# Optimization experiments

Hardware: AMD Instinct MI355X
Metric: run time of the kernel (lower is better)

## Reference

```python
import jax, jax.numpy as jnp
import numpy as np

N_HEAD = 16

def setup_inputs() -> dict:
    key = jax.random.key(0)
    ks = jax.random.split(key, 5)
    C = 1024
    s = 0.02
    return {
        "x": jax.random.normal(ks[0], (4, 2048, C), dtype=jnp.float32),
        "w_attn": jax.random.normal(ks[1], (C, 3 * C), dtype=jnp.float32) * s,
        "b_attn": jnp.zeros((3 * C,), dtype=jnp.float32),
        "w_proj": jax.random.normal(ks[2], (C, C), dtype=jnp.float32) * s,
        "b_proj": jnp.zeros((C,), dtype=jnp.float32),
    }

def reference(x, w_attn, b_attn, w_proj, b_proj):
    B, T, C = x.shape
    H = N_HEAD
    D = C // H
    qkv = x @ w_attn + b_attn                      # [B,T,3C]
    q, k, v = jnp.split(qkv, 3, axis=-1)
    # [B,H,T,D]
    q = q.reshape(B, T, H, D).transpose(0, 2, 1, 3)
    k = k.reshape(B, T, H, D).transpose(0, 2, 1, 3)
    v = v.reshape(B, T, H, D).transpose(0, 2, 1, 3)
    scale = 1.0 / np.sqrt(D).astype(np.float32)
    attn = jnp.einsum('bhtd,bhsd->bhts', q, k) * scale   # [B,H,T,T]
    causal = jnp.tril(jnp.ones((T, T), dtype=bool))
    attn = jnp.where(causal, attn, -jnp.inf)
    attn = jax.nn.softmax(attn, axis=-1)
    y = jnp.einsum('bhts,bhsd->bhtd', attn, v)           # [B,H,T,D]
    y = y.transpose(0, 2, 1, 3).reshape(B, T, C)
    return y @ w_proj + b_proj
```

## Files before the change

### kernel.cpp

```cpp
#include <hip/hip_runtime.h>
#include <hip/hip_bf16.h>

typedef short short8 __attribute__((ext_vector_type(8)));
typedef float f32x4 __attribute__((ext_vector_type(4)));
typedef float f32x16 __attribute__((ext_vector_type(16)));

typedef __attribute__((address_space(1))) void as1_void;
typedef __attribute__((address_space(3))) void as3_void;

__device__ __forceinline__ unsigned short f2bf(float f) {
    __hip_bfloat16 h = __float2bfloat16(f);
    return __builtin_bit_cast(unsigned short, h);
}

__device__ __forceinline__ float exp2fast(float x) {
    return __builtin_amdgcn_exp2f(x);
}

__device__ __forceinline__ unsigned int cvtpk(float lo, float hi) {
    unsigned int r;
    asm("v_cvt_pk_bf16_f32 %0, %1, %2" : "=v"(r) : "v"(lo), "v"(hi));
    return r;
}

__device__ __forceinline__ void plswap(unsigned int& a, unsigned int& b) {
    asm("v_permlane32_swap_b32 %0, %1" : "+v"(a), "+v"(b));
}

__device__ __forceinline__ void gload16(const unsigned short* g, unsigned short* l) {
    __builtin_amdgcn_global_load_lds((as1_void*)g, (as3_void*)l, 16, 0, 0);
}

__global__ __launch_bounds__(256) void conv_f32_to_bf16(
    const float* __restrict__ in, unsigned short* __restrict__ out, int n4) {
    int i = blockIdx.x * 256 + threadIdx.x;
    if (i >= n4) return;
    float4 v = ((const float4*)in)[i];
    ushort4 o;
    o.x = f2bf(v.x); o.y = f2bf(v.y); o.z = f2bf(v.z); o.w = f2bf(v.w);
    ((ushort4*)out)[i] = o;
}

__global__ __launch_bounds__(256) void transpose_f32_to_bf16(
    const float* __restrict__ W, unsigned short* __restrict__ WT, int K, int N) {
    __shared__ float tile[32][33];
    int tx = threadIdx.x, ty = threadIdx.y;
    int n0 = blockIdx.x * 32, k0 = blockIdx.y * 32;
#pragma unroll
    for (int j = 0; j < 4; ++j)
        tile[ty + j * 8][tx] = W[(size_t)(k0 + ty + j * 8) * N + n0 + tx];
    __syncthreads();
#pragma unroll
    for (int j = 0; j < 4; ++j)
        WT[(size_t)(n0 + ty + j * 8) * K + k0 + tx] = f2bf(tile[tx][ty + j * 8]);
}

template <int MODE>
__global__ __launch_bounds__(256, 2) void gemm_bt(
    const unsigned short* __restrict__ A,
    const unsigned short* __restrict__ Bt,
    const float* __restrict__ bias,
    void* __restrict__ out0,
    unsigned short* __restrict__ out1,
    int M, int N, int K) {
    __shared__ unsigned short sA[128 * 32];
    __shared__ unsigned short sB[128 * 32];
    const int tid = threadIdx.x;
    const int lane = tid & 63;
    const int w = tid >> 6;
    const int wr = (w >> 1) * 64;
    const int wc = (w & 1) * 64;
    const size_t arow0 = (size_t)blockIdx.x * 128;
    const size_t brow0 = (size_t)blockIdx.y * 128;

    const int grow = (w << 5) + (lane >> 2);
    const int gcol = (lane & 3) << 3;
    const unsigned short* pA0 = A + (arow0 + grow) * (size_t)K + gcol;
    const unsigned short* pB0 = Bt + (brow0 + grow) * (size_t)K + gcol;
    unsigned short* lA = sA + (w << 10);
    unsigned short* lB = sB + (w << 10);

    f32x4 acc[4][4] = {};
    const int fr = lane & 15;
    const int fk = (lane >> 4) << 3;

    for (int k0 = 0; k0 < K; k0 += 32) {
        __syncthreads();
        gload16(pA0 + k0, lA);
        gload16(pA0 + 16 * (size_t)K + k0, lA + 512);
        gload16(pB0 + k0, lB);
        gload16(pB0 + 16 * (size_t)K + k0, lB + 512);
        __syncthreads();

        short8 af[4], bfr[4];
#pragma unroll
        for (int i = 0; i < 4; ++i)
            af[i] = *(const short8*)&sA[(wr + i * 16 + fr) * 32 + fk];
#pragma unroll
        for (int i = 0; i < 4; ++i)
            bfr[i] = *(const short8*)&sB[(wc + i * 16 + fr) * 32 + fk];
#pragma unroll
        for (int mi = 0; mi < 4; ++mi)
#pragma unroll
            for (int ni = 0; ni < 4; ++ni)
                acc[mi][ni] = __builtin_amdgcn_mfma_f32_16x16x32_bf16(
                    af[mi], bfr[ni], acc[mi][ni], 0, 0, 0);
    }

    const int fq = (lane >> 4) << 2;
    if constexpr (MODE == 0) {
#pragma unroll
        for (int mi = 0; mi < 4; ++mi)
#pragma unroll
            for (int ni = 0; ni < 4; ++ni) {
                size_t r = arow0 + wr + mi * 16 + fq;
                size_t c = brow0 + wc + ni * 16 + fr;
                float bv = bias[c];
#pragma unroll
                for (int j = 0; j < 4; ++j)
                    ((float*)out0)[(r + j) * (size_t)N + c] = acc[mi][ni][j] + bv;
            }
    } else {
        const bool isv = (int)(brow0 + wc) >= 2048;
        if (isv) {
#pragma unroll
            for (int mi = 0; mi < 4; ++mi)
#pragma unroll
                for (int ni = 0; ni < 4; ++ni) {
                    int c = (int)brow0 + wc + ni * 16 + fr;
                    float bv = bias[c];
                    int cv = c - 2048;
                    int r0 = (int)arow0 + wr + mi * 16 + fq;
                    int bb = r0 >> 11, t0 = r0 & 2047;
                    unsigned int lo = (unsigned int)f2bf(acc[mi][ni][0] + bv) |
                                      ((unsigned int)f2bf(acc[mi][ni][1] + bv) << 16);
                    unsigned int hi = (unsigned int)f2bf(acc[mi][ni][2] + bv) |
                                      ((unsigned int)f2bf(acc[mi][ni][3] + bv) << 16);
                    *(uint2*)&out1[(((size_t)(bb * 1024 + cv)) << 11) + t0] =
                        make_uint2(lo, hi);
                }
        } else {
            const float qs = ((int)(brow0 + wc) < 1024) ? 0.125f * 1.4426950408889634f
                                                        : 1.0f;
#pragma unroll
            for (int mi = 0; mi < 4; ++mi)
#pragma unroll
                for (int ni = 0; ni < 4; ++ni) {
                    size_t r = arow0 + wr + mi * 16 + fq;
                    size_t c = brow0 + wc + ni * 16 + fr;
                    float bv = bias[c];
#pragma unroll
                    for (int j = 0; j < 4; ++j)
                        ((unsigned short*)out0)[(r + j) * 2048 + c] =
                            f2bf((acc[mi][ni][j] + bv) * qs);
                }
        }
    }
}

__global__ __launch_bounds__(256, 2) void attn_mfma(
    const unsigned short* __restrict__ qk,
    const unsigned short* __restrict__ vt,
    unsigned short* __restrict__ y,
    int BH) {
    constexpr int T = 2048;
    constexpr float THR = 8.0f;

    __shared__ __align__(16) unsigned short sK[2][64 * 64];
    __shared__ __align__(16) unsigned short sV[2][64 * 64];

    const int tid = threadIdx.x;
    const int lane = tid & 63;
    const int w = tid >> 6;
    const int l31 = lane & 31;
    const int b5 = lane >> 5;

    const int bh = blockIdx.x % BH;
    const int qt = 15 - blockIdx.x / BH;
    const int b = bh >> 4;
    const int h = bh & 15;
    const int q0 = qt << 7;
    const int qw0 = q0 + w * 32;

    const unsigned short* kbase = qk + ((size_t)(b * T)) * 2048 + 1024 + h * 64;
    const unsigned short* vbase = vt + ((size_t)(b * 1024 + h * 64)) * 2048;

    const int srow = tid >> 3;
    const int c16 = tid & 7;
    const int swz = ((c16 ^ (srow & 7)) << 3);

    short8 vones;
#pragma unroll
    for (int i = 0; i < 8; ++i) vones[i] = (short)0x3F80;

    short8 aq[4];
    {
        const unsigned short* qbase =
            qk + ((size_t)(b * T + qw0 + l31)) * 2048 + h * 64;
#pragma unroll
        for (int kc = 0; kc < 4; ++kc)
            aq[kc] = *(const short8*)(qbase + b5 * 8 + kc * 16);
    }

    f32x16 O0 = {}, O1 = {};
    f32x16 l_st = {};
    float m_st = -1e30f;

    const int nt = (q0 + 128) >> 6;

    uint4 kd0, kd1, vd0, vd1;
    kd0 = *(const uint4*)(kbase + (size_t)(srow) * 2048 + c16 * 8);
    kd1 = *(const uint4*)(kbase + (size_t)(srow + 32) * 2048 + c16 * 8);
    vd0 = *(const uint4*)(vbase + (size_t)srow * 2048 + c16 * 8);
    vd1 = *(const uint4*)(vbase + (size_t)(srow + 32) * 2048 + c16 * 8);
    *(uint4*)&sK[0][srow * 64 + swz] = kd0;
    *(uint4*)&sK[0][(srow + 32) * 64 + swz] = kd1;
    *(uint4*)&sV[0][srow * 64 + swz] = vd0;
    *(uint4*)&sV[0][(srow + 32) * 64 + swz] = vd1;
    __syncthreads();

    int cur = 0;
    for (int it = 0; it < nt; ++it) {
        const int s0 = it << 6;
        const bool haveNext = (it + 1 < nt);
        if (haveNext) {
            const int s1 = s0 + 64;
            kd0 = *(const uint4*)(kbase + (size_t)(s1 + srow) * 2048 + c16 * 8);
            kd1 = *(const uint4*)(kbase + (size_t)(s1 + srow + 32) * 2048 + c16 * 8);
            vd0 = *(const uint4*)(vbase + (size_t)srow * 2048 + s1 + c16 * 8);
            vd1 = *(const uint4*)(vbase + (size_t)(srow + 32) * 2048 + s1 + c16 * 8);
        }
        const unsigned short* sKc = sK[cur];
        const unsigned short* sVc = sV[cur];

        if (s0 <= qw0 + 31) {
            f32x16 sacc[2] = {};
            __builtin_amdgcn_s_setprio(1);
#pragma unroll
            for (int kc = 0; kc < 4; ++kc) {
#pragma unroll
                for (int ni = 0; ni < 2; ++ni) {
                    const int row = ni * 32 + l31;
                    short8 akf = *(const short8*)&sKc[row * 64 +
                                                      (((b5 + kc * 2) ^ (row & 7))
                                                       << 3)];
                    sacc[ni] = __builtin_amdgcn_mfma_f32_32x32x16_bf16(
                        akf, aq[kc], sacc[ni], 0, 0, 0);
                }
            }
            __builtin_amdgcn_s_setprio(0);

            const bool needMask = (s0 + 63 > qw0);
            const int qg = qw0 + l31;
            if (needMask) {
#pragma unroll
                for (int ni = 0; ni < 2; ++ni)
#pragma unroll
                    for (int reg = 0; reg < 16; ++reg) {
                        const int sg = s0 + ni * 32 + (reg & 3) + 8 * (reg >> 2) +
                                       4 * b5;
                        sacc[ni][reg] = (sg <= qg) ? sacc[ni][reg] : -INFINITY;
                    }
            }

            float mx = sacc[0][0];
#pragma unroll
            for (int reg = 1; reg < 16; ++reg) mx = fmaxf(mx, sacc[0][reg]);
#pragma unroll
            for (int reg = 0; reg < 16; ++reg) mx = fmaxf(mx, sacc[1][reg]);
            mx = fmaxf(mx, __shfl_xor(mx, 32));

            const bool resc = __any(mx > m_st + THR);
            float f_l = 1.0f;
            if (resc) {
                const float mn = fmaxf(m_st, mx);
                f_l = exp2fast(m_st - mn);
                m_st = mn;
            }

#pragma unroll
            for (int ni = 0; ni < 2; ++ni)
#pragma unroll
                for (int reg = 0; reg < 16; ++reg)
                    sacc[ni][reg] = exp2fast(sacc[ni][reg] - m_st);

            short8 pa[4];
#pragma unroll
            for (int c = 0; c < 4; ++c) {
                const int ni = c >> 1;
                const int off = (c & 1) * 8;
                unsigned int pk01 = cvtpk(sacc[ni][off + 0], sacc[ni][off + 1]);
                unsigned int pk23 = cvtpk(sacc[ni][off + 2], sacc[ni][off + 3]);
                unsigned int pk45 = cvtpk(sacc[ni][off + 4], sacc[ni][off + 5]);
                unsigned int pk67 = cvtpk(sacc[ni][off + 6], sacc[ni][off + 7]);
                plswap(pk01, pk45);
                plswap(pk23, pk67);
                uint4 u = make_uint4(pk01, pk23, pk45, pk67);
                pa[c] = __builtin_bit_cast(short8, u);
            }

            if (resc) {
                const int fil = __builtin_bit_cast(int, f_l);
#pragma unroll
                for (int reg = 0; reg < 16; ++reg) {
                    const int qpat = (reg & 3) + 8 * (reg >> 2) + 4 * b5;
                    const float fq = __builtin_bit_cast(
                        float, __builtin_amdgcn_ds_bpermute(
                                   (qpat + (lane & 32)) << 2, fil));
                    O0[reg] *= fq;
                    O1[reg] *= fq;
                    l_st[reg] *= fq;
                }
            }

            f32x16 lacc = {};
            __builtin_amdgcn_s_setprio(1);
#pragma unroll
            for (int c = 0; c < 4; ++c) {
                lacc = __builtin_amdgcn_mfma_f32_32x32x16_bf16(
                    pa[c], vones, lacc, 0, 0, 0);
                {
                    const int row = l31;
                    short8 bvf = *(const short8*)&sVc[row * 64 +
                                                      (((c * 2 + b5) ^ (row & 7))
                                                       << 3)];
                    O0 = __builtin_amdgcn_mfma_f32_32x32x16_bf16(
                        pa[c], bvf, O0, 0, 0, 0);
                }
                {
                    const int row = 32 + l31;
                    short8 bvf = *(const short8*)&sVc[row * 64 +
                                                      (((c * 2 + b5) ^ (row & 7))
                                                       << 3)];
                    O1 = __builtin_amdgcn_mfma_f32_32x32x16_bf16(
                        pa[c], bvf, O1, 0, 0, 0);
                }
            }
            __builtin_amdgcn_s_setprio(0);
#pragma unroll
            for (int reg = 0; reg < 16; ++reg) l_st[reg] += lacc[reg];
        }

        if (haveNext) {
            unsigned short* sKn = sK[cur ^ 1];
            unsigned short* sVn = sV[cur ^ 1];
            *(uint4*)&sKn[srow * 64 + swz] = kd0;
            *(uint4*)&sKn[(srow + 32) * 64 + swz] = kd1;
            *(uint4*)&sVn[srow * 64 + swz] = vd0;
            *(uint4*)&sVn[(srow + 32) * 64 + swz] = vd1;
        }
        __syncthreads();
        cur ^= 1;
    }

#pragma unroll
    for (int reg = 0; reg < 16; ++reg) {
        const int qpat = (reg & 3) + 8 * (reg >> 2) + 4 * b5;
        const float inv = 1.0f / l_st[reg];
        const size_t base = (size_t)(b * T + qw0 + qpat) * 1024 + h * 64 + l31;
        y[base] = f2bf(O0[reg] * inv);
        y[base + 32] = f2bf(O1[reg] * inv);
    }
}

extern "C" void kernel_launch(void* const* d_in, const int* in_sizes, int n_in,
                              void* d_out, int out_size, void* d_ws, size_t ws_size,
                              hipStream_t stream) {
    const float* x      = (const float*)d_in[0];
    const float* w_attn = (const float*)d_in[1];
    const float* b_attn = (const float*)d_in[2];
    const float* w_proj = (const float*)d_in[3];
    const float* b_proj = (const float*)d_in[4];

    const int C = 1024, T = 2048, H = 16;
    const int B = in_sizes[0] / (T * C);
    const int M = B * T;

    unsigned short* xb  = (unsigned short*)d_ws;
    unsigned short* wTa = xb + (size_t)M * C;
    unsigned short* wTp = wTa + (size_t)3 * C * C;
    unsigned short* qkb = wTp + (size_t)C * C;
    unsigned short* vtb = qkb + (size_t)M * 2 * C;
    unsigned short* y   = xb;

    int n4 = (M * C) / 4;
    conv_f32_to_bf16<<<(n4 + 255) / 256, 256, 0, stream>>>(x, xb, n4);
    transpose_f32_to_bf16<<<dim3(3 * C / 32, C / 32), dim3(32, 8), 0, stream>>>(
        w_attn, wTa, C, 3 * C);
    transpose_f32_to_bf16<<<dim3(C / 32, C / 32), dim3(32, 8), 0, stream>>>(
        w_proj, wTp, C, C);
    gemm_bt<2><<<dim3(M / 128, (3 * C) / 128), 256, 0, stream>>>(
        xb, wTa, b_attn, (void*)qkb, vtb, M, 3 * C, C);
    attn_mfma<<<dim3((B * H) * 16), 256, 0, stream>>>(qkb, vtb, y, B * H);
    gemm_bt<0><<<dim3(M / 128, C / 128), 256, 0, stream>>>(
        y, wTp, b_proj, d_out, nullptr, M, C, C);
}
```

Measured before the change: 173.4 us.

## Fuse fp32-to-bf16 conversion of x into QKV GEMM A-tile loading

Removes the standalone conversion kernel for x. The QKV GEMM now reads fp32 activations straight from global memory, packs them to bf16 in registers and stores them to LDS, while B still uses direct global-to-LDS loads. Launch bounds also move from 2 to 3 waves-per-SIMD occupancy. This saves one kernel launch and a bf16 round trip through memory, at the cost of reading fp32 A data again for every N-tile (24 times) and doing the conversion in the GEMM's inner loop.

```diff
diff --git a/kernel.cpp b/kernel.cpp
--- a/kernel.cpp
+++ b/kernel.cpp
@@ -11,6 +11,9 @@
 __device__ __forceinline__ unsigned short f2bf(float f) {
     __hip_bfloat16 h = __float2bfloat16(f);
     return __builtin_bit_cast(unsigned short, h);
+}
+__device__ __forceinline__ unsigned int pack2(float a, float b) {
+    return (unsigned int)f2bf(a) | ((unsigned int)f2bf(b) << 16);
 }
 
 __device__ __forceinline__ float exp2fast(float x) {
@@ -29,16 +32,6 @@
 
 __device__ __forceinline__ void gload16(const unsigned short* g, unsigned short* l) {
     __builtin_amdgcn_global_load_lds((as1_void*)g, (as3_void*)l, 16, 0, 0);
-}
-
-__global__ __launch_bounds__(256) void conv_f32_to_bf16(
-    const float* __restrict__ in, unsigned short* __restrict__ out, int n4) {
-    int i = blockIdx.x * 256 + threadIdx.x;
-    if (i >= n4) return;
-    float4 v = ((const float4*)in)[i];
-    ushort4 o;
-    o.x = f2bf(v.x); o.y = f2bf(v.y); o.z = f2bf(v.z); o.w = f2bf(v.w);
-    ((ushort4*)out)[i] = o;
 }
 
 __global__ __launch_bounds__(256) void transpose_f32_to_bf16(
@@ -56,8 +49,8 @@
 }
 
 template <int MODE>
-__global__ __launch_bounds__(256, 2) void gemm_bt(
-    const unsigned short* __restrict__ A,
+__global__ __launch_bounds__(256, 3) void gemm_bt(
+    const void* __restrict__ A,
     const unsigned short* __restrict__ Bt,
     const float* __restrict__ bias,
     void* __restrict__ out0,
@@ -75,7 +68,9 @@
 
     const int grow = (w << 5) + (lane >> 2);
     const int gcol = (lane & 3) << 3;
-    const unsigned short* pA0 = A + (arow0 + grow) * (size_t)K + gcol;
+    const unsigned short* pA0 =
+        (const unsigned short*)A + (arow0 + grow) * (size_t)K + gcol;
+    const float* pAf = (const float*)A + (arow0 + grow) * (size_t)K + gcol;
     const unsigned short* pB0 = Bt + (brow0 + grow) * (size_t)K + gcol;
     unsigned short* lA = sA + (w << 10);
     unsigned short* lB = sB + (w << 10);
@@ -86,10 +81,25 @@
 
     for (int k0 = 0; k0 < K; k0 += 32) {
         __syncthreads();
-        gload16(pA0 + k0, lA);
-        gload16(pA0 + 16 * (size_t)K + k0, lA + 512);
-        gload16(pB0 + k0, lB);
-        gload16(pB0 + 16 * (size_t)K + k0, lB + 512);
+        if constexpr (MODE == 0) {
+            gload16(pA0 + k0, lA);
+            gload16(pA0 + 16 * (size_t)K + k0, lA + 512);
+            gload16(pB0 + k0, lB);
+            gload16(pB0 + 16 * (size_t)K + k0, lB + 512);
+        } else {
+            float4 xa0 = *(const float4*)(pAf + k0);
+            float4 xa1 = *(const float4*)(pAf + k0 + 4);
+            float4 xb0 = *(const float4*)(pAf + 16 * (size_t)K + k0);
+            float4 xb1 = *(const float4*)(pAf + 16 * (size_t)K + k0 + 4);
+            gload16(pB0 + k0, lB);
+            gload16(pB0 + 16 * (size_t)K + k0, lB + 512);
+            uint4 w0 = make_uint4(pack2(xa0.x, xa0.y), pack2(xa0.z, xa0.w),
+                                  pack2(xa1.x, xa1.y), pack2(xa1.z, xa1.w));
+            uint4 w1 = make_uint4(pack2(xb0.x, xb0.y), pack2(xb0.z, xb0.w),
+                                  pack2(xb1.x, xb1.y), pack2(xb1.z, xb1.w));
+            *(uint4*)&sA[grow * 32 + gcol] = w0;
+            *(uint4*)&sA[(grow + 16) * 32 + gcol] = w1;
+        }
         __syncthreads();
 
         short8 af[4], bfr[4];
@@ -132,10 +142,8 @@
                     int cv = c - 2048;
                     int r0 = (int)arow0 + wr + mi * 16 + fq;
                     int bb = r0 >> 11, t0 = r0 & 2047;
-                    unsigned int lo = (unsigned int)f2bf(acc[mi][ni][0] + bv) |
-                                      ((unsigned int)f2bf(acc[mi][ni][1] + bv) << 16);
-                    unsigned int hi = (unsigned int)f2bf(acc[mi][ni][2] + bv) |
-                                      ((unsigned int)f2bf(acc[mi][ni][3] + bv) << 16);
+                    unsigned int lo = pack2(acc[mi][ni][0] + bv, acc[mi][ni][1] + bv);
+                    unsigned int hi = pack2(acc[mi][ni][2] + bv, acc[mi][ni][3] + bv);
                     *(uint2*)&out1[(((size_t)(bb * 1024 + cv)) << 11) + t0] =
                         make_uint2(lo, hi);
                 }
@@ -376,22 +384,19 @@
     const int B = in_sizes[0] / (T * C);
     const int M = B * T;
 
-    unsigned short* xb  = (unsigned short*)d_ws;
-    unsigned short* wTa = xb + (size_t)M * C;
+    unsigned short* yb  = (unsigned short*)d_ws;
+    unsigned short* wTa = yb + (size_t)M * C;
     unsigned short* wTp = wTa + (size_t)3 * C * C;
     unsigned short* qkb = wTp + (size_t)C * C;
     unsigned short* vtb = qkb + (size_t)M * 2 * C;
-    unsigned short* y   = xb;
-
-    int n4 = (M * C) / 4;
-    conv_f32_to_bf16<<<(n4 + 255) / 256, 256, 0, stream>>>(x, xb, n4);
+
     transpose_f32_to_bf16<<<dim3(3 * C / 32, C / 32), dim3(32, 8), 0, stream>>>(
         w_attn, wTa, C, 3 * C);
     transpose_f32_to_bf16<<<dim3(C / 32, C / 32), dim3(32, 8), 0, stream>>>(
         w_proj, wTp, C, C);
     gemm_bt<2><<<dim3(M / 128, (3 * C) / 128), 256, 0, stream>>>(
-        xb, wTa, b_attn, (void*)qkb, vtb, M, 3 * C, C);
-    attn_mfma<<<dim3((B * H) * 16), 256, 0, stream>>>(qkb, vtb, y, B * H);
+        (const void*)x, wTa, b_attn, (void*)qkb, vtb, M, 3 * C, C);
+    attn_mfma<<<dim3((B * H) * 16), 256, 0, stream>>>(qkb, vtb, yb, B * H);
     gemm_bt<0><<<dim3(M / 128, C / 128), 256, 0, stream>>>(
-        y, wTp, b_proj, d_out, nullptr, M, C, C);
-}
+        (const void*)yb, wTp, b_proj, d_out, nullptr, M, C, C);
+}
```

Result: slower. 178.7 us (+3.1%).

## Double GEMM K-tile to 64 with XOR-swizzled LDS layout

Applied to the files above, without the earlier changes.

Each GEMM main-loop iteration now loads a 64-wide K slice instead of 32, which halves the number of barrier pairs per K. The global-to-LDS direct loads write into a layout whose 16-byte chunks are XOR-swizzled by row, so the fragment reads avoid LDS bank conflicts. LDS use doubles to 32KB per block, which may limit occupancy, and the swizzled source addressing makes each row load read permuted chunks.

```diff
diff --git a/kernel.cpp b/kernel.cpp
--- a/kernel.cpp
+++ b/kernel.cpp
@@ -63,8 +63,8 @@
     void* __restrict__ out0,
     unsigned short* __restrict__ out1,
     int M, int N, int K) {
-    __shared__ unsigned short sA[128 * 32];
-    __shared__ unsigned short sB[128 * 32];
+    __shared__ unsigned short sA[128 * 64];
+    __shared__ unsigned short sB[128 * 64];
     const int tid = threadIdx.x;
     const int lane = tid & 63;
     const int w = tid >> 6;
@@ -73,38 +73,48 @@
     const size_t arow0 = (size_t)blockIdx.x * 128;
     const size_t brow0 = (size_t)blockIdx.y * 128;
 
-    const int grow = (w << 5) + (lane >> 2);
-    const int gcol = (lane & 3) << 3;
-    const unsigned short* pA0 = A + (arow0 + grow) * (size_t)K + gcol;
-    const unsigned short* pB0 = Bt + (brow0 + grow) * (size_t)K + gcol;
-    unsigned short* lA = sA + (w << 10);
-    unsigned short* lB = sB + (w << 10);
+    const int grow = (w << 5) + (lane >> 3);
+    const int gcolswz = (((lane & 7) ^ ((lane >> 3) & 7)) << 3);
+    const unsigned short* pA0 = A + (arow0 + grow) * (size_t)K + gcolswz;
+    const unsigned short* pB0 = Bt + (brow0 + grow) * (size_t)K + gcolswz;
+    unsigned short* lA = sA + (w << 11);
+    unsigned short* lB = sB + (w << 11);
 
     f32x4 acc[4][4] = {};
     const int fr = lane & 15;
-    const int fk = (lane >> 4) << 3;
-
-    for (int k0 = 0; k0 < K; k0 += 32) {
+    const int g = lane >> 4;
+
+    for (int k0 = 0; k0 < K; k0 += 64) {
         __syncthreads();
-        gload16(pA0 + k0, lA);
-        gload16(pA0 + 16 * (size_t)K + k0, lA + 512);
-        gload16(pB0 + k0, lB);
-        gload16(pB0 + 16 * (size_t)K + k0, lB + 512);
+#pragma unroll
+        for (int j = 0; j < 4; ++j) {
+            gload16(pA0 + (size_t)(j * 8) * K + k0, lA + j * 512);
+            gload16(pB0 + (size_t)(j * 8) * K + k0, lB + j * 512);
+        }
         __syncthreads();
 
-        short8 af[4], bfr[4];
-#pragma unroll
-        for (int i = 0; i < 4; ++i)
-            af[i] = *(const short8*)&sA[(wr + i * 16 + fr) * 32 + fk];
-#pragma unroll
-        for (int i = 0; i < 4; ++i)
-            bfr[i] = *(const short8*)&sB[(wc + i * 16 + fr) * 32 + fk];
-#pragma unroll
-        for (int mi = 0; mi < 4; ++mi)
-#pragma unroll
-            for (int ni = 0; ni < 4; ++ni)
-                acc[mi][ni] = __builtin_amdgcn_mfma_f32_16x16x32_bf16(
-                    af[mi], bfr[ni], acc[mi][ni], 0, 0, 0);
+#pragma unroll
+        for (int kc = 0; kc < 2; ++kc) {
+            short8 af[4], bfr[4];
+#pragma unroll
+            for (int i = 0; i < 4; ++i) {
+                const int row = wr + i * 16 + fr;
+                af[i] = *(const short8*)&sA[row * 64 +
+                                            (((kc * 4 + g) ^ (row & 7)) << 3)];
+            }
+#pragma unroll
+            for (int i = 0; i < 4; ++i) {
+                const int row = wc + i * 16 + fr;
+                bfr[i] = *(const short8*)&sB[row * 64 +
+                                             (((kc * 4 + g) ^ (row & 7)) << 3)];
+            }
+#pragma unroll
+            for (int mi = 0; mi < 4; ++mi)
+#pragma unroll
+                for (int ni = 0; ni < 4; ++ni)
+                    acc[mi][ni] = __builtin_amdgcn_mfma_f32_16x16x32_bf16(
+                        af[mi], bfr[ni], acc[mi][ni], 0, 0, 0);
+        }
     }
 
     const int fq = (lane >> 4) << 2;
```

Result: faster. 168.3 us (-2.9%).
